# Kernel tuning notes

Measured on AMD Instinct MI355X. Metric: run time of the kernel, lower is better.

## Reference

```python
import jax, jax.numpy as jnp
import numpy as np

NUM_DST = 100_000   # blk.num_dst()
E = 1_000_000       # number of temporal edges
U_N = 200_000       # unique node rows
U_E = 100_000       # unique edge-feature rows
U_T = 100_000       # unique time deltas
DN, DE, DT, DOUT, H = 172, 172, 100, 100, 2
NEG_SLOPE = 0.2
LN_EPS = 1e-5


def _lin_init(k, fan_in, fan_out):
    return jax.random.normal(k, (fan_in, fan_out), jnp.float32) / np.float32(np.sqrt(fan_in))


def setup_inputs() -> dict:
    key = jax.random.key(0)
    ks = jax.random.split(key, 16)
    return {
        "nodeData": jax.random.normal(ks[0], (U_N, DN), jnp.float32),
        "efeat_unique": jax.random.normal(ks[1], (U_E, DE), jnp.float32),
        "unique_time_delta": jax.random.uniform(ks[2], (U_T,), jnp.float32) * 1000.0,
        "reverse_nids": jax.random.randint(ks[3], (NUM_DST + E,), 0, U_N, jnp.int32),
        "reverse_eids": jax.random.randint(ks[4], (E,), 0, U_E, jnp.int32),
        "reverse_time_delta": jax.random.randint(ks[5], (E,), 0, U_T, jnp.int32),
        "dstindex": jax.random.randint(ks[6], (E,), 0, NUM_DST, jnp.int32),
        "num_dst": NUM_DST,
        "time_w": jax.random.normal(ks[7], (DT,), jnp.float32),
        "time_b": jax.random.normal(ks[8], (DT,), jnp.float32),
        "Wqn": _lin_init(ks[9], DN, DOUT), "bqn": jnp.zeros((DOUT,), jnp.float32),
        "Wqt": _lin_init(ks[10], DT, DOUT), "bqt": jnp.zeros((DOUT,), jnp.float32),
        "Wkvn": _lin_init(ks[11], DN, 2 * DOUT), "bkvn": jnp.zeros((2 * DOUT,), jnp.float32),
        "Wkve": _lin_init(ks[12], DE, 2 * DOUT), "bkve": jnp.zeros((2 * DOUT,), jnp.float32),
        "Wkvt": _lin_init(ks[13], DT, 2 * DOUT), "bkvt": jnp.zeros((2 * DOUT,), jnp.float32),
        "Wout": _lin_init(ks[14], DN + DOUT, DOUT), "bout": jnp.zeros((DOUT,), jnp.float32),
        "ln_g": jnp.ones((DOUT,), jnp.float32), "ln_b": jnp.zeros((DOUT,), jnp.float32),
    }


def _forward(nodeData, efeat_unique, unique_time_delta, time_w, time_b,
             Wqn, bqn, Wqt, bqt, Wkvn, bkvn, Wkve, bkve, Wkvt, bkvt,
             Wout, bout, ln_g, ln_b,
             reverse_nids, reverse_eids, reverse_time_delta, dstindex, num_dst):
    node_dst_inv = reverse_nids[:num_dst]   # dst -> unique node row
    node_inv = reverse_nids[num_dst:]       # edge -> unique node row (src/nbr)
    # TimeEncode: cos(t * w + b); t=0 for all dst nodes (single shared row).
    nbrs_time_feat = jnp.cos(unique_time_delta[:, None] * time_w[None, :] + time_b[None, :])  # [U_T, DT]
    time_dst = jnp.cos(time_b)[None, :]                                                       # [1, DT]
    # Queries: project unique tables once, then gather (dedup trick).
    q = (nodeData @ Wqn + bqn)[node_dst_inv] + (time_dst @ Wqt + bqt)  # [num_dst, DOUT]
    Q = q[dstindex]                                                    # [E, DOUT]
    # Keys/values: fused node+edge+time projections, gathered per edge.
    Z = ((nodeData @ Wkvn + bkvn)[node_inv]
         + (efeat_unique @ Wkve + bkve)[reverse_eids]
         + (nbrs_time_feat @ Wkvt + bkvt)[reverse_time_delta])         # [E, 2*DOUT]
    dh = DOUT // H
    K = Z[:, :DOUT].reshape(-1, H, dh)
    V = Z[:, DOUT:].reshape(-1, H, dh)
    Qh = Q.reshape(-1, H, dh)
    attn = jax.nn.leaky_relu(jnp.sum(Qh * K, axis=2), NEG_SLOPE)       # [E, H]
    # edge softmax over incoming edges of each dst node
    m = jax.lax.stop_gradient(jax.ops.segment_max(attn, dstindex, num_segments=num_dst))
    e = jnp.exp(attn - m[dstindex])
    s = jax.ops.segment_sum(e, dstindex, num_segments=num_dst)
    a = e / s[dstindex]                                                # [E, H]
    # edge reduce (sum) -> [num_dst, DOUT]
    out = jax.ops.segment_sum((V * a[:, :, None]).reshape(-1, DOUT), dstindex, num_segments=num_dst)
    out = jnp.concatenate([out, nodeData[node_dst_inv]], axis=1)       # [num_dst, DOUT+DN]
    out = jax.nn.relu(out @ Wout + bout)
    mu = out.mean(axis=-1, keepdims=True)
    var = out.var(axis=-1, keepdims=True)
    return (out - mu) / jnp.sqrt(var + LN_EPS) * ln_g + ln_b


def reference(nodeData, efeat_unique, unique_time_delta, reverse_nids, reverse_eids,
              reverse_time_delta, dstindex, num_dst, time_w, time_b,
              Wqn, bqn, Wqt, bqt, Wkvn, bkvn, Wkve, bkve, Wkvt, bkvt,
              Wout, bout, ln_g, ln_b):
    return _forward(nodeData, efeat_unique, unique_time_delta, time_w, time_b,
                    Wqn, bqn, Wqt, bqt, Wkvn, bkvn, Wkve, bkve, Wkvt, bkvt,
                    Wout, bout, ln_g, ln_b,
                    reverse_nids, reverse_eids, reverse_time_delta, dstindex, num_dst)
```

## Files before the change

kernel.cpp:

```cpp
#include <hip/hip_runtime.h>
#include <hip/hip_bf16.h>

typedef __hip_bfloat16 bf16;

#define K_NUM_DST 100000
#define K_E       1000000
#define K_UN      200000
#define K_UE      100000
#define K_UT      100000
#define K_DN      172
#define K_DT      100
#define K_DOUT    100
#define K_DKV     200
#define K_DCAT    272
#define K_MAXE    128
#define K_NEG_SLOPE 0.2f
#define K_LN_EPS    1e-5f

__device__ __forceinline__ float bits2f(unsigned short u){
  union { float f; unsigned int i; } c; c.i = ((unsigned int)u) << 16; return c.f;
}
__device__ __forceinline__ float t2f(float v){ return v; }
__device__ __forceinline__ float t2f(bf16 v){ return __bfloat162float(v); }
__device__ __forceinline__ void store_tab(float* p, float v){ *p = v; }
__device__ __forceinline__ void store_tab(bf16* p, float v){ *p = __float2bfloat16(v); }

template<typename TIN> struct OutStore;
template<> struct OutStore<float>{
  static __device__ __forceinline__ void st(void* o, size_t i, float v){ ((float*)o)[i] = v; }
};
template<> struct OutStore<bf16>{
  static __device__ __forceinline__ void st(void* o, size_t i, float v){ ((bf16*)o)[i] = __float2bfloat16(v); }
};

template<typename TIN> struct Ld4;
template<> struct Ld4<float>{
  static __device__ __forceinline__ float4 ld(const void* base, size_t eo){
    return *(const float4*)((const float*)base + eo);
  }
};
template<> struct Ld4<bf16>{
  static __device__ __forceinline__ float4 ld(const void* base, size_t eo){
    ushort4 u = *(const ushort4*)((const unsigned short*)base + eo);
    float4 f; f.x = bits2f(u.x); f.y = bits2f(u.y); f.z = bits2f(u.z); f.w = bits2f(u.w);
    return f;
  }
};

__global__ void detect_kernel(const unsigned short* __restrict__ nd, int* __restrict__ dflag){
  unsigned int i = blockIdx.x * 256u + threadIdx.x;
  unsigned short u = nd[i];
  if (((u >> 7) & 0xFF) == 0xFF) atomicOr(dflag, 1);
}

template<typename TIN>
__global__ void qt_kernel(const int* __restrict__ dflag, int want,
                          const void* time_b_v, const void* Wqt_v,
                          const void* bqt_v, float* __restrict__ qt){
  if (*dflag != want) return;
  const TIN* time_b = (const TIN*)time_b_v;
  const TIN* Wqt = (const TIN*)Wqt_v;
  const TIN* bqt = (const TIN*)bqt_v;
  int c = threadIdx.x;
  if (c >= K_DOUT) return;
  float acc = t2f(bqt[c]);
  for (int k = 0; k < K_DT; k++)
    acc += cosf(t2f(time_b[k])) * t2f(Wqt[k * K_DOUT + c]);
  qt[c] = acc;
}

template<typename TAB, typename TIN>
__global__ void node_proj_kernel(const int* __restrict__ dflag, int want,
    const void* nodeData_v, const void* Wqn_v, const void* bqn_v,
    const void* Wkvn_v, const void* bkvn_v,
    TAB* __restrict__ qn_tab, TAB* __restrict__ kvn_tab){
  if (*dflag != want) return;
  __shared__ float4 x4[16][43];
  int row0 = blockIdx.x * 16;
  int tid = threadIdx.x;
  for (int idx = tid; idx < 16 * 43; idx += 320){
    int r = idx / 43, kk = idx - r * 43;
    x4[r][kk] = Ld4<TIN>::ld(nodeData_v, (size_t)(row0 + r) * K_DN + kk * 4);
  }
  __syncthreads();
  int c = tid;
  if (c >= 300) return;
  const TIN* W = (c < K_DOUT) ? (const TIN*)Wqn_v : (const TIN*)Wkvn_v;
  int ldw = (c < K_DOUT) ? K_DOUT : K_DKV;
  int cc  = (c < K_DOUT) ? c : c - K_DOUT;
  float acc[16];
  #pragma unroll
  for (int r = 0; r < 16; r++) acc[r] = 0.f;
  for (int kk = 0; kk < 43; kk++){
    float w0 = t2f(W[(kk*4+0)*ldw + cc]);
    float w1 = t2f(W[(kk*4+1)*ldw + cc]);
    float w2 = t2f(W[(kk*4+2)*ldw + cc]);
    float w3 = t2f(W[(kk*4+3)*ldw + cc]);
    #pragma unroll
    for (int r = 0; r < 16; r++){
      float4 xv = x4[r][kk];
      acc[r] = fmaf(xv.x, w0, acc[r]);
      acc[r] = fmaf(xv.y, w1, acc[r]);
      acc[r] = fmaf(xv.z, w2, acc[r]);
      acc[r] = fmaf(xv.w, w3, acc[r]);
    }
  }
  float bias = t2f((c < K_DOUT) ? ((const TIN*)bqn_v)[cc] : ((const TIN*)bkvn_v)[cc]);
  if (c < K_DOUT){
    #pragma unroll
    for (int r = 0; r < 16; r++) store_tab(&qn_tab[(size_t)(row0+r)*K_DOUT + cc], acc[r] + bias);
  } else {
    #pragma unroll
    for (int r = 0; r < 16; r++) store_tab(&kvn_tab[(size_t)(row0+r)*K_DKV + cc], acc[r] + bias);
  }
}

template<typename TAB, typename TIN>
__global__ void feat_proj_kernel(const int* __restrict__ dflag, int want,
    const void* A_v, const void* W_v, const void* bias_v,
    TAB* __restrict__ out_tab){
  if (*dflag != want) return;
  __shared__ float4 x4[16][43];
  int row0 = blockIdx.x * 16;
  int tid = threadIdx.x;
  for (int idx = tid; idx < 16 * 43; idx += 256){
    int r = idx / 43, kk = idx - r * 43;
    x4[r][kk] = Ld4<TIN>::ld(A_v, (size_t)(row0 + r) * K_DN + kk * 4);
  }
  __syncthreads();
  int c = tid;
  if (c >= K_DKV) return;
  const TIN* W = (const TIN*)W_v;
  float acc[16];
  #pragma unroll
  for (int r = 0; r < 16; r++) acc[r] = 0.f;
  for (int kk = 0; kk < 43; kk++){
    float w0 = t2f(W[(kk*4+0)*K_DKV + c]);
    float w1 = t2f(W[(kk*4+1)*K_DKV + c]);
    float w2 = t2f(W[(kk*4+2)*K_DKV + c]);
    float w3 = t2f(W[(kk*4+3)*K_DKV + c]);
    #pragma unroll
    for (int r = 0; r < 16; r++){
      float4 xv = x4[r][kk];
      acc[r] = fmaf(xv.x, w0, acc[r]);
      acc[r] = fmaf(xv.y, w1, acc[r]);
      acc[r] = fmaf(xv.z, w2, acc[r]);
      acc[r] = fmaf(xv.w, w3, acc[r]);
    }
  }
  float bb = t2f(((const TIN*)bias_v)[c]);
  #pragma unroll
  for (int r = 0; r < 16; r++)
    store_tab(&out_tab[(size_t)(row0+r)*K_DKV + c], acc[r] + bb);
}

template<typename TAB, typename TIN>
__global__ void time_proj_kernel(const int* __restrict__ dflag, int want,
    const void* utd_v, const void* time_w_v, const void* time_b_v,
    const void* Wkvt_v, const void* bkvt_v,
    TAB* __restrict__ kvt_tab){
  if (*dflag != want) return;
  __shared__ float xs[16][K_DT];
  __shared__ float ts[16];
  int row0 = blockIdx.x * 16;
  int tid = threadIdx.x;
  if (tid < 16) ts[tid] = t2f(((const TIN*)utd_v)[row0 + tid]);
  __syncthreads();
  for (int idx = tid; idx < 16 * K_DT; idx += 256){
    int r = idx / K_DT, k = idx - r * K_DT;
    xs[r][k] = cosf(ts[r] * t2f(((const TIN*)time_w_v)[k]) + t2f(((const TIN*)time_b_v)[k]));
  }
  __syncthreads();
  int c = tid;
  if (c >= K_DKV) return;
  const TIN* W = (const TIN*)Wkvt_v;
  float acc[16];
  #pragma unroll
  for (int r = 0; r < 16; r++) acc[r] = 0.f;
  for (int kk = 0; kk < 25; kk++){
    float w0 = t2f(W[(kk*4+0)*K_DKV + c]);
    float w1 = t2f(W[(kk*4+1)*K_DKV + c]);
    float w2 = t2f(W[(kk*4+2)*K_DKV + c]);
    float w3 = t2f(W[(kk*4+3)*K_DKV + c]);
    #pragma unroll
    for (int r = 0; r < 16; r++){
      float4 xv = ((const float4*)xs[r])[kk];
      acc[r] = fmaf(xv.x, w0, acc[r]);
      acc[r] = fmaf(xv.y, w1, acc[r]);
      acc[r] = fmaf(xv.z, w2, acc[r]);
      acc[r] = fmaf(xv.w, w3, acc[r]);
    }
  }
  float bb = t2f(((const TIN*)bkvt_v)[c]);
  #pragma unroll
  for (int r = 0; r < 16; r++)
    store_tab(&kvt_tab[(size_t)(row0+r)*K_DKV + c], acc[r] + bb);
}

__global__ void hist_kernel(const int* __restrict__ dstindex, int* __restrict__ counts){
  int e = blockIdx.x * blockDim.x + threadIdx.x;
  if (e < K_E) atomicAdd(&counts[dstindex[e]], 1);
}

__global__ void scan1_kernel(const int* __restrict__ counts, int* __restrict__ offsets,
                             int* __restrict__ bsum, int n){
  __shared__ int sd[256];
  int b = blockIdx.x, t = threadIdx.x;
  int base = b * 1024 + t * 4;
  int v0=0,v1=0,v2=0,v3=0;
  if (base+0 < n) v0 = counts[base+0];
  if (base+1 < n) v1 = counts[base+1];
  if (base+2 < n) v2 = counts[base+2];
  if (base+3 < n) v3 = counts[base+3];
  int s = v0+v1+v2+v3;
  sd[t] = s;
  __syncthreads();
  for (int off = 1; off < 256; off <<= 1){
    int tmp = (t >= off) ? sd[t-off] : 0;
    __syncthreads();
    sd[t] += tmp;
    __syncthreads();
  }
  int excl = sd[t] - s;
  if (base+0 < n) offsets[base+0] = excl;
  if (base+1 < n) offsets[base+1] = excl + v0;
  if (base+2 < n) offsets[base+2] = excl + v0 + v1;
  if (base+3 < n) offsets[base+3] = excl + v0 + v1 + v2;
  if (t == 255) bsum[b] = sd[255];
}

__global__ void scan2_kernel(int* bsum, int nb){
  if (threadIdx.x == 0 && blockIdx.x == 0){
    int run = 0;
    for (int i = 0; i < nb; i++){ int v = bsum[i]; bsum[i] = run; run += v; }
  }
}

__global__ void scan3_kernel(int* __restrict__ offsets, const int* __restrict__ bsum, int n){
  int i = blockIdx.x * blockDim.x + threadIdx.x;
  if (i < n) offsets[i] += bsum[i >> 10];
}

__global__ void scatter_kernel(const int* __restrict__ dstindex, const int* __restrict__ offsets,
                               int* __restrict__ cursor, int* __restrict__ edge_ids){
  int e = blockIdx.x * blockDim.x + threadIdx.x;
  if (e < K_E){
    int d = dstindex[e];
    int p = atomicAdd(&cursor[d], 1);
    edge_ids[offsets[d] + p] = e;
  }
}

template<typename TAB>
__global__ void attn_kernel(
    const int* __restrict__ reverse_nids, const int* __restrict__ reverse_eids,
    const int* __restrict__ reverse_tids,
    const int* __restrict__ dstoff, const int* __restrict__ dstcnt,
    const int* __restrict__ edge_ids,
    const TAB* __restrict__ qn_tab, const TAB* __restrict__ kvn_tab,
    const TAB* __restrict__ kve_tab, const TAB* __restrict__ kvt_tab,
    const float* __restrict__ qt, float* __restrict__ out_agg){
  __shared__ int   ids[K_MAXE * 3];
  __shared__ float at[K_MAXE * 2];
  int dst = blockIdx.x;
  int l = threadIdx.x;
  int h = l >> 5, li = l & 31;
  int d0 = 50 * h + li;
  bool d1v = (li < 18);
  int d1 = d0 + 32;
  int start = dstoff[dst];
  int cnt = dstcnt[dst];
  if (cnt > K_MAXE) cnt = K_MAXE;
  int gn = reverse_nids[dst];
  float q0 = t2f(qn_tab[(size_t)gn * K_DOUT + d0]) + qt[d0];
  float q1 = d1v ? (t2f(qn_tab[(size_t)gn * K_DOUT + d1]) + qt[d1]) : 0.f;
  float m = -3.0e38f;
  for (int i = 0; i < cnt; i++){
    int e = edge_ids[start + i];
    int nid = reverse_nids[K_NUM_DST + e];
    int eid = reverse_eids[e];
    int tde = reverse_tids[e];
    if (l == 0){ ids[i*3] = nid; ids[i*3+1] = eid; ids[i*3+2] = tde; }
    float p = q0 * (t2f(kvn_tab[(size_t)nid*K_DKV + d0]) + t2f(kve_tab[(size_t)eid*K_DKV + d0]) + t2f(kvt_tab[(size_t)tde*K_DKV + d0]));
    if (d1v)
      p += q1 * (t2f(kvn_tab[(size_t)nid*K_DKV + d1]) + t2f(kve_tab[(size_t)eid*K_DKV + d1]) + t2f(kvt_tab[(size_t)tde*K_DKV + d1]));
    #pragma unroll
    for (int off = 16; off; off >>= 1) p += __shfl_xor(p, off, 32);
    float a = (p > 0.f) ? p : K_NEG_SLOPE * p;
    if (li == 0) at[i*2 + h] = a;
    m = fmaxf(m, a);
  }
  __syncthreads();
  float s = 0.f;
  for (int i = 0; i < cnt; i++) s += expf(at[i*2 + h] - m);
  float inv_s = (cnt > 0) ? 1.f / s : 0.f;
  float acc0 = 0.f, acc1 = 0.f;
  for (int i = 0; i < cnt; i++){
    int nid = ids[i*3], eid = ids[i*3+1], tde = ids[i*3+2];
    float w = expf(at[i*2 + h] - m) * inv_s;
    acc0 += w * (t2f(kvn_tab[(size_t)nid*K_DKV + K_DOUT + d0]) + t2f(kve_tab[(size_t)eid*K_DKV + K_DOUT + d0]) + t2f(kvt_tab[(size_t)tde*K_DKV + K_DOUT + d0]));
    if (d1v)
      acc1 += w * (t2f(kvn_tab[(size_t)nid*K_DKV + K_DOUT + d1]) + t2f(kve_tab[(size_t)eid*K_DKV + K_DOUT + d1]) + t2f(kvt_tab[(size_t)tde*K_DKV + K_DOUT + d1]));
  }
  out_agg[(size_t)dst * K_DOUT + d0] = acc0;
  if (d1v) out_agg[(size_t)dst * K_DOUT + d1] = acc1;
}

template<typename TIN>
__global__ void final_kernel(const int* __restrict__ dflag, int want,
    const float* __restrict__ out_agg,
    const void* nodeData_v, const int* __restrict__ reverse_nids,
    const void* Wout_v, const void* bout_v,
    const void* ln_g_v, const void* ln_b_v,
    void* out){
  if (*dflag != want) return;
  const TIN* Wout = (const TIN*)Wout_v; const TIN* bout = (const TIN*)bout_v;
  const TIN* ln_g = (const TIN*)ln_g_v; const TIN* ln_b = (const TIN*)ln_b_v;
  __shared__ float x[16][K_DCAT];
  __shared__ float y[16][K_DOUT];
  __shared__ float stats[16][2];
  __shared__ int gnid[16];
  int dbase = blockIdx.x * 16;
  int tid = threadIdx.x;
  if (tid < 16) gnid[tid] = reverse_nids[dbase + tid];
  __syncthreads();
  for (int idx = tid; idx < 16 * 68; idx += 128){
    int r = idx / 68, kk = idx - r * 68;
    float4 v;
    if (kk < 25) v = *(const float4*)(out_agg + (size_t)(dbase + r) * K_DOUT + kk * 4);
    else         v = Ld4<TIN>::ld(nodeData_v, (size_t)gnid[r] * K_DN + (kk - 25) * 4);
    *(float4*)&x[r][kk * 4] = v;
  }
  __syncthreads();
  int c = tid;
  float acc[16];
  #pragma unroll
  for (int r = 0; r < 16; r++) acc[r] = 0.f;
  if (c < K_DOUT){
    for (int kk = 0; kk < 68; kk++){
      float w0 = t2f(Wout[(kk*4+0)*K_DOUT + c]);
      float w1 = t2f(Wout[(kk*4+1)*K_DOUT + c]);
      float w2 = t2f(Wout[(kk*4+2)*K_DOUT + c]);
      float w3 = t2f(Wout[(kk*4+3)*K_DOUT + c]);
      #pragma unroll
      for (int r = 0; r < 16; r++){
        float4 xv = ((const float4*)x[r])[kk];
        acc[r] = fmaf(xv.x, w0, acc[r]);
        acc[r] = fmaf(xv.y, w1, acc[r]);
        acc[r] = fmaf(xv.z, w2, acc[r]);
        acc[r] = fmaf(xv.w, w3, acc[r]);
      }
    }
    float bias = t2f(bout[c]);
    #pragma unroll
    for (int r = 0; r < 16; r++){ acc[r] = fmaxf(acc[r] + bias, 0.f); y[r][c] = acc[r]; }
  }
  __syncthreads();
  {
    int r = tid >> 3, q = tid & 7;
    float s1 = 0.f, s2 = 0.f;
    for (int cc = q; cc < K_DOUT; cc += 8){ float v = y[r][cc]; s1 += v; s2 += v * v; }
    #pragma unroll
    for (int off = 4; off; off >>= 1){ s1 += __shfl_xor(s1, off, 8); s2 += __shfl_xor(s2, off, 8); }
    if (q == 0){ stats[r][0] = s1; stats[r][1] = s2; }
  }
  __syncthreads();
  if (c < K_DOUT){
    float g = t2f(ln_g[c]), bb = t2f(ln_b[c]);
    #pragma unroll
    for (int r = 0; r < 16; r++){
      float mu = stats[r][0] * (1.f / K_DOUT);
      float var = stats[r][1] * (1.f / K_DOUT) - mu * mu;
      float v = (acc[r] - mu) * rsqrtf(var + K_LN_EPS) * g + bb;
      OutStore<TIN>::st(out, (size_t)(dbase + r) * K_DOUT + c, v);
    }
  }
}

static inline size_t al256(size_t b){ return (b + 255) & ~(size_t)255; }

template<typename TAB>
static void run_pipeline(void* const* d_in, void* out, char* ws, hipStream_t stream){
  const void* nodeData = d_in[0];
  const void* efeat    = d_in[1];
  const void* utd      = d_in[2];
  const int* reverse_nids = (const int*)d_in[3];
  const int* reverse_eids = (const int*)d_in[4];
  const int* reverse_tids = (const int*)d_in[5];
  const int* dstindex     = (const int*)d_in[6];
  const void* time_w = d_in[8];
  const void* time_b = d_in[9];
  const void* Wqn  = d_in[10]; const void* bqn  = d_in[11];
  const void* Wqt  = d_in[12]; const void* bqt  = d_in[13];
  const void* Wkvn = d_in[14]; const void* bkvn = d_in[15];
  const void* Wkve = d_in[16]; const void* bkve = d_in[17];
  const void* Wkvt = d_in[18]; const void* bkvt = d_in[19];
  const void* Wout = d_in[20]; const void* bout = d_in[21];
  const void* ln_g = d_in[22]; const void* ln_b = d_in[23];

  char* p = ws;
  int* dflag = (int*)p;       p += 256;
  TAB* qn_tab  = (TAB*)p; p += al256(sizeof(TAB) * (size_t)K_UN * K_DOUT);
  TAB* kvn_tab = (TAB*)p; p += al256(sizeof(TAB) * (size_t)K_UN * K_DKV);
  TAB* kve_tab = (TAB*)p; p += al256(sizeof(TAB) * (size_t)K_UE * K_DKV);
  TAB* kvt_tab = (TAB*)p; p += al256(sizeof(TAB) * (size_t)K_UT * K_DKV);
  float* out_agg = (float*)p; p += al256(sizeof(float) * (size_t)K_NUM_DST * K_DOUT);
  float* qt = (float*)p;      p += al256(sizeof(float) * K_DOUT);
  int* counts = (int*)p;      p += al256(sizeof(int) * K_NUM_DST);
  int* offsets = (int*)p;     p += al256(sizeof(int) * K_NUM_DST);
  int* cursor = (int*)p;      p += al256(sizeof(int) * K_NUM_DST);
  int* bsum = (int*)p;        p += al256(sizeof(int) * 512);
  int* edge_ids = (int*)p;    p += al256(sizeof(int) * (size_t)K_E);

  hipMemsetAsync(dflag, 0, 256, stream);
  hipMemsetAsync(counts, 0, sizeof(int) * K_NUM_DST, stream);
  hipMemsetAsync(cursor, 0, sizeof(int) * K_NUM_DST, stream);

  detect_kernel<<<512, 256, 0, stream>>>((const unsigned short*)nodeData, dflag);

  qt_kernel<float><<<1, 128, 0, stream>>>(dflag, 1, time_b, Wqt, bqt, qt);
  node_proj_kernel<TAB, float><<<K_UN / 16, 320, 0, stream>>>(dflag, 1, nodeData, Wqn, bqn, Wkvn, bkvn, qn_tab, kvn_tab);
  feat_proj_kernel<TAB, float><<<K_UE / 16, 256, 0, stream>>>(dflag, 1, efeat, Wkve, bkve, kve_tab);
  time_proj_kernel<TAB, float><<<K_UT / 16, 256, 0, stream>>>(dflag, 1, utd, time_w, time_b, Wkvt, bkvt, kvt_tab);
  qt_kernel<bf16><<<1, 128, 0, stream>>>(dflag, 0, time_b, Wqt, bqt, qt);
  node_proj_kernel<TAB, bf16><<<K_UN / 16, 320, 0, stream>>>(dflag, 0, nodeData, Wqn, bqn, Wkvn, bkvn, qn_tab, kvn_tab);
  feat_proj_kernel<TAB, bf16><<<K_UE / 16, 256, 0, stream>>>(dflag, 0, efeat, Wkve, bkve, kve_tab);
  time_proj_kernel<TAB, bf16><<<K_UT / 16, 256, 0, stream>>>(dflag, 0, utd, time_w, time_b, Wkvt, bkvt, kvt_tab);

  hist_kernel<<<(K_E + 255) / 256, 256, 0, stream>>>(dstindex, counts);
  int nb = (K_NUM_DST + 1023) / 1024;
  scan1_kernel<<<nb, 256, 0, stream>>>(counts, offsets, bsum, K_NUM_DST);
  scan2_kernel<<<1, 1, 0, stream>>>(bsum, nb);
  scan3_kernel<<<(K_NUM_DST + 255) / 256, 256, 0, stream>>>(offsets, bsum, K_NUM_DST);
  scatter_kernel<<<(K_E + 255) / 256, 256, 0, stream>>>(dstindex, offsets, cursor, edge_ids);

  attn_kernel<TAB><<<K_NUM_DST, 64, 0, stream>>>(reverse_nids, reverse_eids, reverse_tids,
      offsets, counts, edge_ids, qn_tab, kvn_tab, kve_tab, kvt_tab, qt, out_agg);

  final_kernel<float><<<K_NUM_DST / 16, 128, 0, stream>>>(dflag, 1, out_agg, nodeData, reverse_nids,
      Wout, bout, ln_g, ln_b, out);
  final_kernel<bf16><<<K_NUM_DST / 16, 128, 0, stream>>>(dflag, 0, out_agg, nodeData, reverse_nids,
      Wout, bout, ln_g, ln_b, out);
}

extern "C" void kernel_launch(void* const* d_in, const int* in_sizes, int n_in,
                              void* d_out, int out_size, void* d_ws, size_t ws_size,
                              hipStream_t stream){
  (void)in_sizes; (void)n_in; (void)out_size;

  size_t fixed = 256 + al256(4ull * K_NUM_DST * K_DOUT) + al256(4 * K_DOUT)
               + 3 * al256(4 * K_NUM_DST) + al256(4 * 512) + al256(4ull * K_E);
  size_t tab_elems = (size_t)K_UN * K_DOUT + (size_t)K_UN * K_DKV
                   + (size_t)K_UE * K_DKV + (size_t)K_UT * K_DKV;
  size_t need_f32  = fixed + tab_elems * 4 + 8192;
  size_t need_bf16 = fixed + tab_elems * 2 + 8192;

  if (ws_size >= need_f32){
    run_pipeline<float>(d_in, d_out, (char*)d_ws, stream);
  } else if (ws_size >= need_bf16){
    run_pipeline<bf16>(d_in, d_out, (char*)d_ws, stream);
  }
}
```

Before: 1.787 ms.

## Register-tile projection GEMMs and rewrite attention with single-pass online softmax

```diff
diff --git a/kernel.cpp b/kernel.cpp
--- a/kernel.cpp
+++ b/kernel.cpp
@@ -13,7 +13,6 @@
 #define K_DOUT    100
 #define K_DKV     200
 #define K_DCAT    272
-#define K_MAXE    128
 #define K_NEG_SLOPE 0.2f
 #define K_LN_EPS    1e-5f
 
@@ -22,8 +21,6 @@
 }
 __device__ __forceinline__ float t2f(float v){ return v; }
 __device__ __forceinline__ float t2f(bf16 v){ return __bfloat162float(v); }
-__device__ __forceinline__ void store_tab(float* p, float v){ *p = v; }
-__device__ __forceinline__ void store_tab(bf16* p, float v){ *p = __float2bfloat16(v); }
 
 template<typename TIN> struct OutStore;
 template<> struct OutStore<float>{
@@ -46,6 +43,14 @@
     return f;
   }
 };
+
+template<typename TAB> __device__ __forceinline__ void store4(TAB* p, float a, float b, float c, float d);
+template<> __device__ __forceinline__ void store4<float>(float* p, float a, float b, float c, float d){
+  float4 v; v.x=a; v.y=b; v.z=c; v.w=d; *(float4*)p = v;
+}
+template<> __device__ __forceinline__ void store4<bf16>(bf16* p, float a, float b, float c, float d){
+  p[0]=__float2bfloat16(a); p[1]=__float2bfloat16(b); p[2]=__float2bfloat16(c); p[3]=__float2bfloat16(d);
+}
 
 __global__ void detect_kernel(const unsigned short* __restrict__ nd, int* __restrict__ dflag){
   unsigned int i = blockIdx.x * 256u + threadIdx.x;
@@ -70,131 +75,120 @@
 }
 
 template<typename TAB, typename TIN>
-__global__ void node_proj_kernel(const int* __restrict__ dflag, int want,
+__global__ __launch_bounds__(320)
+void node_proj_kernel(const int* __restrict__ dflag, int want,
     const void* nodeData_v, const void* Wqn_v, const void* bqn_v,
     const void* Wkvn_v, const void* bkvn_v,
     TAB* __restrict__ qn_tab, TAB* __restrict__ kvn_tab){
   if (*dflag != want) return;
-  __shared__ float4 x4[16][43];
+  __shared__ float xT[K_DN][20];
   int row0 = blockIdx.x * 16;
   int tid = threadIdx.x;
   for (int idx = tid; idx < 16 * 43; idx += 320){
-    int r = idx / 43, kk = idx - r * 43;
-    x4[r][kk] = Ld4<TIN>::ld(nodeData_v, (size_t)(row0 + r) * K_DN + kk * 4);
-  }
-  __syncthreads();
-  int c = tid;
-  if (c >= 300) return;
-  const TIN* W = (c < K_DOUT) ? (const TIN*)Wqn_v : (const TIN*)Wkvn_v;
-  int ldw = (c < K_DOUT) ? K_DOUT : K_DKV;
-  int cc  = (c < K_DOUT) ? c : c - K_DOUT;
-  float acc[16];
+    int r = idx / 43, kk = idx % 43;
+    float4 v = Ld4<TIN>::ld(nodeData_v, (size_t)(row0 + r) * K_DN + kk * 4);
+    xT[kk*4+0][r] = v.x; xT[kk*4+1][r] = v.y; xT[kk*4+2][r] = v.z; xT[kk*4+3][r] = v.w;
+  }
+  __syncthreads();
+  if (tid >= 300) return;
+  int ci = tid % 75, ri = tid / 75;
+  const void* W; const TIN* B; int ldw, c0;
+  if (ci < 25){ W = Wqn_v;  B = (const TIN*)bqn_v;  ldw = K_DOUT; c0 = 4*ci; }
+  else        { W = Wkvn_v; B = (const TIN*)bkvn_v; ldw = K_DKV;  c0 = 4*(ci-25); }
+  float acc[4][4] = {};
+  #pragma unroll 4
+  for (int k = 0; k < K_DN; k++){
+    float4 a = *(const float4*)&xT[k][4*ri];
+    float4 w = Ld4<TIN>::ld(W, (size_t)k * ldw + c0);
+    acc[0][0]=fmaf(a.x,w.x,acc[0][0]); acc[0][1]=fmaf(a.x,w.y,acc[0][1]); acc[0][2]=fmaf(a.x,w.z,acc[0][2]); acc[0][3]=fmaf(a.x,w.w,acc[0][3]);
+    acc[1][0]=fmaf(a.y,w.x,acc[1][0]); acc[1][1]=fmaf(a.y,w.y,acc[1][1]); acc[1][2]=fmaf(a.y,w.z,acc[1][2]); acc[1][3]=fmaf(a.y,w.w,acc[1][3]);
+    acc[2][0]=fmaf(a.z,w.x,acc[2][0]); acc[2][1]=fmaf(a.z,w.y,acc[2][1]); acc[2][2]=fmaf(a.z,w.z,acc[2][2]); acc[2][3]=fmaf(a.z,w.w,acc[2][3]);
+    acc[3][0]=fmaf(a.w,w.x,acc[3][0]); acc[3][1]=fmaf(a.w,w.y,acc[3][1]); acc[3][2]=fmaf(a.w,w.z,acc[3][2]); acc[3][3]=fmaf(a.w,w.w,acc[3][3]);
+  }
+  float b0 = t2f(B[c0+0]), b1 = t2f(B[c0+1]), b2 = t2f(B[c0+2]), b3 = t2f(B[c0+3]);
+  TAB* tab = (ci < 25) ? qn_tab : kvn_tab;
   #pragma unroll
-  for (int r = 0; r < 16; r++) acc[r] = 0.f;
-  for (int kk = 0; kk < 43; kk++){
-    float w0 = t2f(W[(kk*4+0)*ldw + cc]);
-    float w1 = t2f(W[(kk*4+1)*ldw + cc]);
-    float w2 = t2f(W[(kk*4+2)*ldw + cc]);
-    float w3 = t2f(W[(kk*4+3)*ldw + cc]);
-    #pragma unroll
-    for (int r = 0; r < 16; r++){
-      float4 xv = x4[r][kk];
-      acc[r] = fmaf(xv.x, w0, acc[r]);
-      acc[r] = fmaf(xv.y, w1, acc[r]);
-      acc[r] = fmaf(xv.z, w2, acc[r]);
-      acc[r] = fmaf(xv.w, w3, acc[r]);
-    }
-  }
-  float bias = t2f((c < K_DOUT) ? ((const TIN*)bqn_v)[cc] : ((const TIN*)bkvn_v)[cc]);
-  if (c < K_DOUT){
-    #pragma unroll
-    for (int r = 0; r < 16; r++) store_tab(&qn_tab[(size_t)(row0+r)*K_DOUT + cc], acc[r] + bias);
-  } else {
-    #pragma unroll
-    for (int r = 0; r < 16; r++) store_tab(&kvn_tab[(size_t)(row0+r)*K_DKV + cc], acc[r] + bias);
+  for (int i = 0; i < 4; i++){
+    size_t row = row0 + 4*ri + i;
+    store4<TAB>(&tab[row * ldw + c0], acc[i][0]+b0, acc[i][1]+b1, acc[i][2]+b2, acc[i][3]+b3);
   }
 }
 
 template<typename TAB, typename TIN>
-__global__ void feat_proj_kernel(const int* __restrict__ dflag, int want,
+__global__ __launch_bounds__(256)
+void feat_proj_kernel(const int* __restrict__ dflag, int want,
     const void* A_v, const void* W_v, const void* bias_v,
     TAB* __restrict__ out_tab){
   if (*dflag != want) return;
-  __shared__ float4 x4[16][43];
-  int row0 = blockIdx.x * 16;
+  __shared__ float xT[K_DN][20];
+  int row0 = blockIdx.x * 20;
   int tid = threadIdx.x;
-  for (int idx = tid; idx < 16 * 43; idx += 256){
-    int r = idx / 43, kk = idx - r * 43;
-    x4[r][kk] = Ld4<TIN>::ld(A_v, (size_t)(row0 + r) * K_DN + kk * 4);
-  }
-  __syncthreads();
-  int c = tid;
-  if (c >= K_DKV) return;
-  const TIN* W = (const TIN*)W_v;
-  float acc[16];
+  for (int idx = tid; idx < 20 * 43; idx += 256){
+    int r = idx / 43, kk = idx % 43;
+    float4 v = Ld4<TIN>::ld(A_v, (size_t)(row0 + r) * K_DN + kk * 4);
+    xT[kk*4+0][r] = v.x; xT[kk*4+1][r] = v.y; xT[kk*4+2][r] = v.z; xT[kk*4+3][r] = v.w;
+  }
+  __syncthreads();
+  if (tid >= 250) return;
+  int ci = tid % 50, ri = tid / 50;
+  int c0 = 4 * ci;
+  float acc[4][4] = {};
+  #pragma unroll 4
+  for (int k = 0; k < K_DN; k++){
+    float4 a = *(const float4*)&xT[k][4*ri];
+    float4 w = Ld4<TIN>::ld(W_v, (size_t)k * K_DKV + c0);
+    acc[0][0]=fmaf(a.x,w.x,acc[0][0]); acc[0][1]=fmaf(a.x,w.y,acc[0][1]); acc[0][2]=fmaf(a.x,w.z,acc[0][2]); acc[0][3]=fmaf(a.x,w.w,acc[0][3]);
+    acc[1][0]=fmaf(a.y,w.x,acc[1][0]); acc[1][1]=fmaf(a.y,w.y,acc[1][1]); acc[1][2]=fmaf(a.y,w.z,acc[1][2]); acc[1][3]=fmaf(a.y,w.w,acc[1][3]);
+    acc[2][0]=fmaf(a.z,w.x,acc[2][0]); acc[2][1]=fmaf(a.z,w.y,acc[2][1]); acc[2][2]=fmaf(a.z,w.z,acc[2][2]); acc[2][3]=fmaf(a.z,w.w,acc[2][3]);
+    acc[3][0]=fmaf(a.w,w.x,acc[3][0]); acc[3][1]=fmaf(a.w,w.y,acc[3][1]); acc[3][2]=fmaf(a.w,w.z,acc[3][2]); acc[3][3]=fmaf(a.w,w.w,acc[3][3]);
+  }
+  const TIN* B = (const TIN*)bias_v;
+  float b0 = t2f(B[c0+0]), b1 = t2f(B[c0+1]), b2 = t2f(B[c0+2]), b3 = t2f(B[c0+3]);
   #pragma unroll
-  for (int r = 0; r < 16; r++) acc[r] = 0.f;
-  for (int kk = 0; kk < 43; kk++){
-    float w0 = t2f(W[(kk*4+0)*K_DKV + c]);
-    float w1 = t2f(W[(kk*4+1)*K_DKV + c]);
-    float w2 = t2f(W[(kk*4+2)*K_DKV + c]);
-    float w3 = t2f(W[(kk*4+3)*K_DKV + c]);
-    #pragma unroll
-    for (int r = 0; r < 16; r++){
-      float4 xv = x4[r][kk];
-      acc[r] = fmaf(xv.x, w0, acc[r]);
-      acc[r] = fmaf(xv.y, w1, acc[r]);
-      acc[r] = fmaf(xv.z, w2, acc[r]);
-      acc[r] = fmaf(xv.w, w3, acc[r]);
-    }
-  }
-  float bb = t2f(((const TIN*)bias_v)[c]);
-  #pragma unroll
-  for (int r = 0; r < 16; r++)
-    store_tab(&out_tab[(size_t)(row0+r)*K_DKV + c], acc[r] + bb);
+  for (int i = 0; i < 4; i++){
+    size_t row = row0 + 4*ri + i;
+    store4<TAB>(&out_tab[row * K_DKV + c0], acc[i][0]+b0, acc[i][1]+b1, acc[i][2]+b2, acc[i][3]+b3);
+  }
 }
 
 template<typename TAB, typename TIN>
-__global__ void time_proj_kernel(const int* __restrict__ dflag, int want,
+__global__ __launch_bounds__(256)
+void time_proj_kernel(const int* __restrict__ dflag, int want,
     const void* utd_v, const void* time_w_v, const void* time_b_v,
     const void* Wkvt_v, const void* bkvt_v,
     TAB* __restrict__ kvt_tab){
   if (*dflag != want) return;
-  __shared__ float xs[16][K_DT];
-  __shared__ float ts[16];
-  int row0 = blockIdx.x * 16;
+  __shared__ float xT[K_DT][20];
+  __shared__ float ts[20];
+  int row0 = blockIdx.x * 20;
   int tid = threadIdx.x;
-  if (tid < 16) ts[tid] = t2f(((const TIN*)utd_v)[row0 + tid]);
-  __syncthreads();
-  for (int idx = tid; idx < 16 * K_DT; idx += 256){
-    int r = idx / K_DT, k = idx - r * K_DT;
-    xs[r][k] = cosf(ts[r] * t2f(((const TIN*)time_w_v)[k]) + t2f(((const TIN*)time_b_v)[k]));
-  }
-  __syncthreads();
-  int c = tid;
-  if (c >= K_DKV) return;
-  const TIN* W = (const TIN*)Wkvt_v;
-  float acc[16];
+  if (tid < 20) ts[tid] = t2f(((const TIN*)utd_v)[row0 + tid]);
+  __syncthreads();
+  for (int idx = tid; idx < 20 * K_DT; idx += 256){
+    int r = idx / K_DT, k = idx % K_DT;
+    xT[k][r] = cosf(ts[r] * t2f(((const TIN*)time_w_v)[k]) + t2f(((const TIN*)time_b_v)[k]));
+  }
+  __syncthreads();
+  if (tid >= 250) return;
+  int ci = tid % 50, ri = tid / 50;
+  int c0 = 4 * ci;
+  float acc[4][4] = {};
+  #pragma unroll 4
+  for (int k = 0; k < K_DT; k++){
+    float4 a = *(const float4*)&xT[k][4*ri];
+    float4 w = Ld4<TIN>::ld(Wkvt_v, (size_t)k * K_DKV + c0);
+    acc[0][0]=fmaf(a.x,w.x,acc[0][0]); acc[0][1]=fmaf(a.x,w.y,acc[0][1]); acc[0][2]=fmaf(a.x,w.z,acc[0][2]); acc[0][3]=fmaf(a.x,w.w,acc[0][3]);
+    acc[1][0]=fmaf(a.y,w.x,acc[1][0]); acc[1][1]=fmaf(a.y,w.y,acc[1][1]); acc[1][2]=fmaf(a.y,w.z,acc[1][2]); acc[1][3]=fmaf(a.y,w.w,acc[1][3]);
+    acc[2][0]=fmaf(a.z,w.x,acc[2][0]); acc[2][1]=fmaf(a.z,w.y,acc[2][1]); acc[2][2]=fmaf(a.z,w.z,acc[2][2]); acc[2][3]=fmaf(a.z,w.w,acc[2][3]);
+    acc[3][0]=fmaf(a.w,w.x,acc[3][0]); acc[3][1]=fmaf(a.w,w.y,acc[3][1]); acc[3][2]=fmaf(a.w,w.z,acc[3][2]); acc[3][3]=fmaf(a.w,w.w,acc[3][3]);
+  }
+  const TIN* B = (const TIN*)bkvt_v;
+  float b0 = t2f(B[c0+0]), b1 = t2f(B[c0+1]), b2 = t2f(B[c0+2]), b3 = t2f(B[c0+3]);
   #pragma unroll
-  for (int r = 0; r < 16; r++) acc[r] = 0.f;
-  for (int kk = 0; kk < 25; kk++){
-    float w0 = t2f(W[(kk*4+0)*K_DKV + c]);
-    float w1 = t2f(W[(kk*4+1)*K_DKV + c]);
-    float w2 = t2f(W[(kk*4+2)*K_DKV + c]);
-    float w3 = t2f(W[(kk*4+3)*K_DKV + c]);
-    #pragma unroll
-    for (int r = 0; r < 16; r++){
-      float4 xv = ((const float4*)xs[r])[kk];
-      acc[r] = fmaf(xv.x, w0, acc[r]);
-      acc[r] = fmaf(xv.y, w1, acc[r]);
-      acc[r] = fmaf(xv.z, w2, acc[r]);
-      acc[r] = fmaf(xv.w, w3, acc[r]);
-    }
-  }
-  float bb = t2f(((const TIN*)bkvt_v)[c]);
-  #pragma unroll
-  for (int r = 0; r < 16; r++)
-    store_tab(&kvt_tab[(size_t)(row0+r)*K_DKV + c], acc[r] + bb);
+  for (int i = 0; i < 4; i++){
+    size_t row = row0 + 4*ri + i;
+    store4<TAB>(&kvt_tab[row * K_DKV + c0], acc[i][0]+b0, acc[i][1]+b1, acc[i][2]+b2, acc[i][3]+b3);
+  }
 }
 
 __global__ void hist_kernel(const int* __restrict__ dstindex, int* __restrict__ counts){
@@ -252,7 +246,8 @@
 }
 
 template<typename TAB>
-__global__ void attn_kernel(
+__global__ __launch_bounds__(256)
+void attn_kernel(
     const int* __restrict__ reverse_nids, const int* __restrict__ reverse_eids,
     const int* __restrict__ reverse_tids,
     const int* __restrict__ dstoff, const int* __restrict__ dstcnt,
@@ -260,119 +255,170 @@
     const TAB* __restrict__ qn_tab, const TAB* __restrict__ kvn_tab,
     const TAB* __restrict__ kve_tab, const TAB* __restrict__ kvt_tab,
     const float* __restrict__ qt, float* __restrict__ out_agg){
-  __shared__ int   ids[K_MAXE * 3];
-  __shared__ float at[K_MAXE * 2];
-  int dst = blockIdx.x;
-  int l = threadIdx.x;
-  int h = l >> 5, li = l & 31;
-  int d0 = 50 * h + li;
-  bool d1v = (li < 18);
-  int d1 = d0 + 32;
+  int tid = threadIdx.x;
+  int wave = tid >> 6;
+  int l = tid & 63;
+  int h = l >> 5;
+  int li = l & 31;
+  int dst = blockIdx.x * 4 + wave;
   int start = dstoff[dst];
   int cnt = dstcnt[dst];
-  if (cnt > K_MAXE) cnt = K_MAXE;
+  int cntw = (cnt + 1 - h) >> 1;
+  bool act = (li < 25);
+  int d4 = 4 * li;
+  bool c0h0 = (d4+0) < 50, c1h0 = (d4+1) < 50, c2h0 = (d4+2) < 50, c3h0 = (d4+3) < 50;
+
   int gn = reverse_nids[dst];
-  float q0 = t2f(qn_tab[(size_t)gn * K_DOUT + d0]) + qt[d0];
-  float q1 = d1v ? (t2f(qn_tab[(size_t)gn * K_DOUT + d1]) + qt[d1]) : 0.f;
-  float m = -3.0e38f;
-  for (int i = 0; i < cnt; i++){
-    int e = edge_ids[start + i];
+  float4 q = make_float4(0.f,0.f,0.f,0.f);
+  if (act){
+    float4 qn = Ld4<TAB>::ld(qn_tab, (size_t)gn * K_DOUT + d4);
+    float4 qtv = *(const float4*)(qt + d4);
+    q.x = qn.x + qtv.x; q.y = qn.y + qtv.y; q.z = qn.z + qtv.z; q.w = qn.w + qtv.w;
+  }
+
+  float m0 = -3.0e38f, m1 = -3.0e38f, s0 = 0.f, s1 = 0.f;
+  float ax = 0.f, ay = 0.f, az = 0.f, aw = 0.f;
+
+  for (int j = 0; j < cntw; j++){
+    int e   = edge_ids[start + 2*j + h];
     int nid = reverse_nids[K_NUM_DST + e];
     int eid = reverse_eids[e];
     int tde = reverse_tids[e];
-    if (l == 0){ ids[i*3] = nid; ids[i*3+1] = eid; ids[i*3+2] = tde; }
-    float p = q0 * (t2f(kvn_tab[(size_t)nid*K_DKV + d0]) + t2f(kve_tab[(size_t)eid*K_DKV + d0]) + t2f(kvt_tab[(size_t)tde*K_DKV + d0]));
-    if (d1v)
-      p += q1 * (t2f(kvn_tab[(size_t)nid*K_DKV + d1]) + t2f(kve_tab[(size_t)eid*K_DKV + d1]) + t2f(kvt_tab[(size_t)tde*K_DKV + d1]));
+    float4 kx = make_float4(0.f,0.f,0.f,0.f);
+    if (act){
+      float4 k1 = Ld4<TAB>::ld(kvn_tab, (size_t)nid * K_DKV + d4);
+      float4 k2 = Ld4<TAB>::ld(kve_tab, (size_t)eid * K_DKV + d4);
+      float4 k3 = Ld4<TAB>::ld(kvt_tab, (size_t)tde * K_DKV + d4);
+      kx.x = k1.x+k2.x+k3.x; kx.y = k1.y+k2.y+k3.y; kx.z = k1.z+k2.z+k3.z; kx.w = k1.w+k2.w+k3.w;
+    }
+    float px = q.x*kx.x, py = q.y*kx.y, pz = q.z*kx.z, pw = q.w*kx.w;
+    float p0 = (c0h0?px:0.f) + (c1h0?py:0.f) + (c2h0?pz:0.f) + (c3h0?pw:0.f);
+    float p1 = (px+py+pz+pw) - p0;
     #pragma unroll
-    for (int off = 16; off; off >>= 1) p += __shfl_xor(p, off, 32);
-    float a = (p > 0.f) ? p : K_NEG_SLOPE * p;
-    if (li == 0) at[i*2 + h] = a;
-    m = fmaxf(m, a);
-  }
-  __syncthreads();
-  float s = 0.f;
-  for (int i = 0; i < cnt; i++) s += expf(at[i*2 + h] - m);
-  float inv_s = (cnt > 0) ? 1.f / s : 0.f;
-  float acc0 = 0.f, acc1 = 0.f;
-  for (int i = 0; i < cnt; i++){
-    int nid = ids[i*3], eid = ids[i*3+1], tde = ids[i*3+2];
-    float w = expf(at[i*2 + h] - m) * inv_s;
-    acc0 += w * (t2f(kvn_tab[(size_t)nid*K_DKV + K_DOUT + d0]) + t2f(kve_tab[(size_t)eid*K_DKV + K_DOUT + d0]) + t2f(kvt_tab[(size_t)tde*K_DKV + K_DOUT + d0]));
-    if (d1v)
-      acc1 += w * (t2f(kvn_tab[(size_t)nid*K_DKV + K_DOUT + d1]) + t2f(kve_tab[(size_t)eid*K_DKV + K_DOUT + d1]) + t2f(kvt_tab[(size_t)tde*K_DKV + K_DOUT + d1]));
-  }
-  out_agg[(size_t)dst * K_DOUT + d0] = acc0;
-  if (d1v) out_agg[(size_t)dst * K_DOUT + d1] = acc1;
+    for (int off = 16; off; off >>= 1){
+      p0 += __shfl_xor(p0, off);
+      p1 += __shfl_xor(p1, off);
+    }
+    float a0 = (p0 > 0.f) ? p0 : K_NEG_SLOPE * p0;
+    float a1 = (p1 > 0.f) ? p1 : K_NEG_SLOPE * p1;
+    float nm0 = fmaxf(m0, a0), nm1 = fmaxf(m1, a1);
+    float al0 = __expf(m0 - nm0), al1 = __expf(m1 - nm1);
+    float e0  = __expf(a0 - nm0), e1  = __expf(a1 - nm1);
+    s0 = s0 * al0 + e0; s1 = s1 * al1 + e1;
+    m0 = nm0; m1 = nm1;
+    float4 vx = make_float4(0.f,0.f,0.f,0.f);
+    if (act){
+      float4 v1 = Ld4<TAB>::ld(kvn_tab, (size_t)nid * K_DKV + K_DOUT + d4);
+      float4 v2 = Ld4<TAB>::ld(kve_tab, (size_t)eid * K_DKV + K_DOUT + d4);
+      float4 v3 = Ld4<TAB>::ld(kvt_tab, (size_t)tde * K_DKV + K_DOUT + d4);
+      vx.x = v1.x+v2.x+v3.x; vx.y = v1.y+v2.y+v3.y; vx.z = v1.z+v2.z+v3.z; vx.w = v1.w+v2.w+v3.w;
+    }
+    ax = ax * (c0h0?al0:al1) + (c0h0?e0:e1) * vx.x;
+    ay = ay * (c1h0?al0:al1) + (c1h0?e0:e1) * vx.y;
+    az = az * (c2h0?al0:al1) + (c2h0?e0:e1) * vx.z;
+    aw = aw * (c3h0?al0:al1) + (c3h0?e0:e1) * vx.w;
+  }
+
+  float mo0 = __shfl_xor(m0, 32), so0 = __shfl_xor(s0, 32);
+  float mo1 = __shfl_xor(m1, 32), so1 = __shfl_xor(s1, 32);
+  float aox = __shfl_xor(ax, 32), aoy = __shfl_xor(ay, 32);
+  float aoz = __shfl_xor(az, 32), aow = __shfl_xor(aw, 32);
+  float M0 = fmaxf(m0, mo0), M1 = fmaxf(m1, mo1);
+  float cs0 = __expf(m0 - M0), co0 = __expf(mo0 - M0);
+  float cs1 = __expf(m1 - M1), co1 = __expf(mo1 - M1);
+  float S0 = s0 * cs0 + so0 * co0;
+  float S1 = s1 * cs1 + so1 * co1;
+  float inv0 = (S0 > 0.f) ? 1.f / S0 : 0.f;
+  float inv1 = (S1 > 0.f) ? 1.f / S1 : 0.f;
+  float rx = c0h0 ? (ax*cs0 + aox*co0)*inv0 : (ax*cs1 + aox*co1)*inv1;
+  float ry = c1h0 ? (ay*cs0 + aoy*co0)*inv0 : (ay*cs1 + aoy*co1)*inv1;
+  float rz = c2h0 ? (az*cs0 + aoz*co0)*inv0 : (az*cs1 + aoz*co1)*inv1;
+  float rw = c3h0 ? (aw*cs0 + aow*co0)*inv0 : (aw*cs1 + aow*co1)*inv1;
+  if (h == 0 && act){
+    float4 r; r.x=rx; r.y=ry; r.z=rz; r.w=rw;
+    *(float4*)(out_agg + (size_t)dst * K_DOUT + d4) = r;
+  }
 }
 
 template<typename TIN>
-__global__ void final_kernel(const int* __restrict__ dflag, int want,
+__global__ __launch_bounds__(256)
+void final_kernel(const int* __restrict__ dflag, int want,
     const float* __restrict__ out_agg,
     const void* nodeData_v, const int* __restrict__ reverse_nids,
     const void* Wout_v, const void* bout_v,
     const void* ln_g_v, const void* ln_b_v,
     void* out){
   if (*dflag != want) return;
-  const TIN* Wout = (const TIN*)Wout_v; const TIN* bout = (const TIN*)bout_v;
-  const TIN* ln_g = (const TIN*)ln_g_v; const TIN* ln_b = (const TIN*)ln_b_v;
-  __shared__ float x[16][K_DCAT];
-  __shared__ float y[16][K_DOUT];
-  __shared__ float stats[16][2];
-  __shared__ int gnid[16];
-  int dbase = blockIdx.x * 16;
+  __shared__ float xT[K_DCAT][36];
+  __shared__ float y[32][104];
+  __shared__ float stats[32][2];
+  __shared__ int gnid[32];
+  int dbase = blockIdx.x * 32;
   int tid = threadIdx.x;
-  if (tid < 16) gnid[tid] = reverse_nids[dbase + tid];
-  __syncthreads();
-  for (int idx = tid; idx < 16 * 68; idx += 128){
-    int r = idx / 68, kk = idx - r * 68;
-    float4 v;
-    if (kk < 25) v = *(const float4*)(out_agg + (size_t)(dbase + r) * K_DOUT + kk * 4);
-    else         v = Ld4<TIN>::ld(nodeData_v, (size_t)gnid[r] * K_DN + (kk - 25) * 4);
-    *(float4*)&x[r][kk * 4] = v;
-  }
-  __syncthreads();
-  int c = tid;
-  float acc[16];
-  #pragma unroll
-  for (int r = 0; r < 16; r++) acc[r] = 0.f;
-  if (c < K_DOUT){
-    for (int kk = 0; kk < 68; kk++){
-      float w0 = t2f(Wout[(kk*4+0)*K_DOUT + c]);
-      float w1 = t2f(Wout[(kk*4+1)*K_DOUT + c]);
-      float w2 = t2f(Wout[(kk*4+2)*K_DOUT + c]);
-      float w3 = t2f(Wout[(kk*4+3)*K_DOUT + c]);
-      #pragma unroll
-      for (int r = 0; r < 16; r++){
-        float4 xv = ((const float4*)x[r])[kk];
-        acc[r] = fmaf(xv.x, w0, acc[r]);
-        acc[r] = fmaf(xv.y, w1, acc[r]);
-        acc[r] = fmaf(xv.z, w2, acc[r]);
-        acc[r] = fmaf(xv.w, w3, acc[r]);
-      }
+  if (tid < 32) gnid[tid] = reverse_nids[dbase + tid];
+  __syncthreads();
+  for (int idx = tid; idx < 32 * 25; idx += 256){
+    int r = idx / 25, kk = idx % 25;
+    float4 v = *(const float4*)(out_agg + (size_t)(dbase + r) * K_DOUT + kk * 4);
+    xT[kk*4+0][r] = v.x; xT[kk*4+1][r] = v.y; xT[kk*4+2][r] = v.z; xT[kk*4+3][r] = v.w;
+  }
+  for (int idx = tid; idx < 32 * 43; idx += 256){
+    int r = idx / 43, kk = idx % 43;
+    float4 v = Ld4<TIN>::ld(nodeData_v, (size_t)gnid[r] * K_DN + kk * 4);
+    xT[K_DOUT + kk*4+0][r] = v.x; xT[K_DOUT + kk*4+1][r] = v.y;
+    xT[K_DOUT + kk*4+2][r] = v.z; xT[K_DOUT + kk*4+3][r] = v.w;
+  }
+  __syncthreads();
+  int ci = tid % 25, ri = tid / 25;
+  float acc[4][4] = {};
+  int c0 = 4 * ci;
+  if (tid < 200){
+    #pragma unroll 4
+    for (int k = 0; k < K_DCAT; k++){
+      float4 a = *(const float4*)&xT[k][4*ri];
+      float4 w = Ld4<TIN>::ld(Wout_v, (size_t)k * K_DOUT + c0);
+      acc[0][0]=fmaf(a.x,w.x,acc[0][0]); acc[0][1]=fmaf(a.x,w.y,acc[0][1]); acc[0][2]=fmaf(a.x,w.z,acc[0][2]); acc[0][3]=fmaf(a.x,w.w,acc[0][3]);
+      acc[1][0]=fmaf(a.y,w.x,acc[1][0]); acc[1][1]=fmaf(a.y,w.y,acc[1][1]); acc[1][2]=fmaf(a.y,w.z,acc[1][2]); acc[1][3]=fmaf(a.y,w.w,acc[1][3]);
+      acc[2][0]=fmaf(a.z,w.x,acc[2][0]); acc[2][1]=fmaf(a.z,w.y,acc[2][1]); acc[2][2]=fmaf(a.z,w.z,acc[2][2]); acc[2][3]=fmaf(a.z,w.w,acc[2][3]);
+      acc[3][0]=fmaf(a.w,w.x,acc[3][0]); acc[3][1]=fmaf(a.w,w.y,acc[3][1]); acc[3][2]=fmaf(a.w,w.z,acc[3][2]); acc[3][3]=fmaf(a.w,w.w,acc[3][3]);
     }
-    float bias = t2f(bout[c]);
+    const TIN* B = (const TIN*)bout_v;
+    float b0 = t2f(B[c0+0]), b1 = t2f(B[c0+1]), b2 = t2f(B[c0+2]), b3 = t2f(B[c0+3]);
     #pragma unroll
-    for (int r = 0; r < 16; r++){ acc[r] = fmaxf(acc[r] + bias, 0.f); y[r][c] = acc[r]; }
+    for (int i = 0; i < 4; i++){
+      acc[i][0] = fmaxf(acc[i][0]+b0, 0.f);
+      acc[i][1] = fmaxf(acc[i][1]+b1, 0.f);
+      acc[i][2] = fmaxf(acc[i][2]+b2, 0.f);
+      acc[i][3] = fmaxf(acc[i][3]+b3, 0.f);
+      float4 v; v.x=acc[i][0]; v.y=acc[i][1]; v.z=acc[i][2]; v.w=acc[i][3];
+      *(float4*)&y[4*ri + i][c0] = v;
+    }
   }
   __syncthreads();
   {
-    int r = tid >> 3, q = tid & 7;
+    int r = tid >> 3, qq = tid & 7;
     float s1 = 0.f, s2 = 0.f;
-    for (int cc = q; cc < K_DOUT; cc += 8){ float v = y[r][cc]; s1 += v; s2 += v * v; }
+    for (int cc = qq; cc < K_DOUT; cc += 8){ float v = y[r][cc]; s1 += v; s2 += v * v; }
     #pragma unroll
     for (int off = 4; off; off >>= 1){ s1 += __shfl_xor(s1, off, 8); s2 += __shfl_xor(s2, off, 8); }
-    if (q == 0){ stats[r][0] = s1; stats[r][1] = s2; }
-  }
-  __syncthreads();
-  if (c < K_DOUT){
-    float g = t2f(ln_g[c]), bb = t2f(ln_b[c]);
+    if (qq == 0){ stats[r][0] = s1; stats[r][1] = s2; }
+  }
+  __syncthreads();
+  if (tid < 200){
+    const TIN* G = (const TIN*)ln_g_v; const TIN* Bb = (const TIN*)ln_b_v;
+    float g0 = t2f(G[c0+0]), g1 = t2f(G[c0+1]), g2 = t2f(G[c0+2]), g3 = t2f(G[c0+3]);
+    float lb0 = t2f(Bb[c0+0]), lb1 = t2f(Bb[c0+1]), lb2 = t2f(Bb[c0+2]), lb3 = t2f(Bb[c0+3]);
     #pragma unroll
-    for (int r = 0; r < 16; r++){
+    for (int i = 0; i < 4; i++){
+      int r = 4*ri + i;
       float mu = stats[r][0] * (1.f / K_DOUT);
       float var = stats[r][1] * (1.f / K_DOUT) - mu * mu;
-      float v = (acc[r] - mu) * rsqrtf(var + K_LN_EPS) * g + bb;
-      OutStore<TIN>::st(out, (size_t)(dbase + r) * K_DOUT + c, v);
+      float rs = rsqrtf(var + K_LN_EPS);
+      size_t o = (size_t)(dbase + r) * K_DOUT + c0;
+      OutStore<TIN>::st(out, o+0, (acc[i][0]-mu)*rs*g0 + lb0);
+      OutStore<TIN>::st(out, o+1, (acc[i][1]-mu)*rs*g1 + lb1);
+      OutStore<TIN>::st(out, o+2, (acc[i][2]-mu)*rs*g2 + lb2);
+      OutStore<TIN>::st(out, o+3, (acc[i][3]-mu)*rs*g3 + lb3);
     }
   }
 }
@@ -420,12 +466,12 @@
 
   qt_kernel<float><<<1, 128, 0, stream>>>(dflag, 1, time_b, Wqt, bqt, qt);
   node_proj_kernel<TAB, float><<<K_UN / 16, 320, 0, stream>>>(dflag, 1, nodeData, Wqn, bqn, Wkvn, bkvn, qn_tab, kvn_tab);
-  feat_proj_kernel<TAB, float><<<K_UE / 16, 256, 0, stream>>>(dflag, 1, efeat, Wkve, bkve, kve_tab);
-  time_proj_kernel<TAB, float><<<K_UT / 16, 256, 0, stream>>>(dflag, 1, utd, time_w, time_b, Wkvt, bkvt, kvt_tab);
+  feat_proj_kernel<TAB, float><<<K_UE / 20, 256, 0, stream>>>(dflag, 1, efeat, Wkve, bkve, kve_tab);
+  time_proj_kernel<TAB, float><<<K_UT / 20, 256, 0, stream>>>(dflag, 1, utd, time_w, time_b, Wkvt, bkvt, kvt_tab);
   qt_kernel<bf16><<<1, 128, 0, stream>>>(dflag, 0, time_b, Wqt, bqt, qt);
   node_proj_kernel<TAB, bf16><<<K_UN / 16, 320, 0, stream>>>(dflag, 0, nodeData, Wqn, bqn, Wkvn, bkvn, qn_tab, kvn_tab);
-  feat_proj_kernel<TAB, bf16><<<K_UE / 16, 256, 0, stream>>>(dflag, 0, efeat, Wkve, bkve, kve_tab);
-  time_proj_kernel<TAB, bf16><<<K_UT / 16, 256, 0, stream>>>(dflag, 0, utd, time_w, time_b, Wkvt, bkvt, kvt_tab);
+  feat_proj_kernel<TAB, bf16><<<K_UE / 20, 256, 0, stream>>>(dflag, 0, efeat, Wkve, bkve, kve_tab);
+  time_proj_kernel<TAB, bf16><<<K_UT / 20, 256, 0, stream>>>(dflag, 0, utd, time_w, time_b, Wkvt, bkvt, kvt_tab);
 
   hist_kernel<<<(K_E + 255) / 256, 256, 0, stream>>>(dstindex, counts);
   int nb = (K_NUM_DST + 1023) / 1024;
@@ -434,12 +480,12 @@
   scan3_kernel<<<(K_NUM_DST + 255) / 256, 256, 0, stream>>>(offsets, bsum, K_NUM_DST);
   scatter_kernel<<<(K_E + 255) / 256, 256, 0, stream>>>(dstindex, offsets, cursor, edge_ids);
 
-  attn_kernel<TAB><<<K_NUM_DST, 64, 0, stream>>>(reverse_nids, reverse_eids, reverse_tids,
+  attn_kernel<TAB><<<K_NUM_DST / 4, 256, 0, stream>>>(reverse_nids, reverse_eids, reverse_tids,
       offsets, counts, edge_ids, qn_tab, kvn_tab, kve_tab, kvt_tab, qt, out_agg);
 
-  final_kernel<float><<<K_NUM_DST / 16, 128, 0, stream>>>(dflag, 1, out_agg, nodeData, reverse_nids,
+  final_kernel<float><<<K_NUM_DST / 32, 256, 0, stream>>>(dflag, 1, out_agg, nodeData, reverse_nids,
       Wout, bout, ln_g, ln_b, out);
-  final_kernel<bf16><<<K_NUM_DST / 16, 128, 0, stream>>>(dflag, 0, out_agg, nodeData, reverse_nids,
+  final_kernel<bf16><<<K_NUM_DST / 32, 256, 0, stream>>>(dflag, 0, out_agg, nodeData, reverse_nids,
       Wout, bout, ln_g, ln_b, out);
 }
 
```

Measured after the change: 1.732 ms. 3.0% less time.
